# Performance work log

Measured on AMD Instinct MI355X. Metric: run time of the kernel, lower is better.

## Reference

```python
import jax, jax.numpy as jnp
import numpy as np

B = 4
C = 128           # input channels
H = W = 512       # image size
P = 16            # patch size
GH = GW = 32      # token grid (H//P, W//P)
N = GH * GW       # num patches = 1024
PATCH_DIM = C * P * P  # 32768
DIM = 512         # embed dim
MLP = 256         # ffn hidden
DH = 64           # dim per head
HEADS = (2, 4, 8) # per-layer head counts
NUM_REL = (2 * GH - 1) * (2 * GW - 1)  # 3969


def _rel_index():
    # faithful to the torch buffer construction (meshgrid default 'ij')
    coords = np.stack(np.meshgrid(np.arange(GH), np.arange(GW), indexing='ij')).reshape(2, -1)
    rc = (coords[:, :, None] - coords[:, None, :]).transpose(1, 2, 0)  # [N,N,2]
    rc[..., 0] += GH - 1
    rc[..., 1] += GW - 1
    rc[..., 0] *= 2 * GH - 1
    return jnp.asarray(rc.sum(-1))  # [N,N] int

REL_IDX = _rel_index()


def _ln(x, s, b):
    m = x.mean(-1, keepdims=True)
    v = x.var(-1, keepdims=True)
    return (x - m) / jnp.sqrt(v + 1e-5) * s + b


def setup_inputs() -> dict:
    key = jax.random.key(0)
    ks = iter(jax.random.split(key, 40))
    def rn(shape, scale=0.02):
        return jax.random.normal(next(ks), shape, jnp.float32) * scale
    inp = {"img": jax.random.normal(next(ks), (B, C, H, W), jnp.float32)}
    inp["patch_w"] = rn((PATCH_DIM, DIM))
    inp["patch_b"] = jnp.zeros((DIM,), jnp.float32)
    inp["pos_emb"] = rn((1, N, DIM), 1.0)
    inp["ln1_s"] = jnp.ones((3, DIM), jnp.float32)
    inp["ln1_b"] = jnp.zeros((3, DIM), jnp.float32)
    inp["ln2_s"] = jnp.ones((3, DIM), jnp.float32)
    inp["ln2_b"] = jnp.zeros((3, DIM), jnp.float32)
    for l, h in enumerate(HEADS):
        inner = DH * h
        inp[f"qkv_w{l}"] = rn((DIM, 3 * inner))
        inp[f"out_w{l}"] = rn((inner, DIM))
        inp[f"out_b{l}"] = jnp.zeros((DIM,), jnp.float32)
        inp[f"bias{l}"] = rn((NUM_REL, h))
    inp["ff_w1"] = rn((3, DIM, MLP))
    inp["ff_b1"] = jnp.zeros((3, MLP), jnp.float32)
    inp["ff_w2"] = rn((3, MLP, DIM))
    inp["ff_b2"] = jnp.zeros((3, DIM), jnp.float32)
    return inp


def reference(img, patch_w, patch_b, pos_emb, ln1_s, ln1_b, ln2_s, ln2_b,
              qkv_w0, qkv_w1, qkv_w2, out_w0, out_w1, out_w2,
              out_b0, out_b1, out_b2, bias0, bias1, bias2,
              ff_w1, ff_b1, ff_w2, ff_b2):
    b = img.shape[0]
    # Rearrange 'b c (h p1) (w p2) -> b (h w) (p1 p2 c)'
    x = img.reshape(b, C, GH, P, GW, P).transpose(0, 2, 4, 3, 5, 1).reshape(b, N, PATCH_DIM)
    x = x @ patch_w + patch_b + pos_emb

    qkv_ws = (qkv_w0, qkv_w1, qkv_w2)
    out_ws = (out_w0, out_w1, out_w2)
    out_bs = (out_b0, out_b1, out_b2)
    tables = (bias0, bias1, bias2)

    for l, h in enumerate(HEADS):
        # attention with relative position bias
        xn = _ln(x, ln1_s[l], ln1_b[l])
        qkv = xn @ qkv_ws[l]                                  # [b, N, 3*h*DH]
        q, k, v = jnp.split(qkv, 3, axis=-1)
        q = q.reshape(b, N, h, DH).transpose(0, 2, 1, 3)      # bhnd
        k = k.reshape(b, N, h, DH).transpose(0, 2, 1, 3)
        v = v.reshape(b, N, h, DH).transpose(0, 2, 1, 3)
        dots = jnp.einsum('bhnd,bhmd->bhnm', q, k) * (DH ** -0.5)
        rel = tables[l][REL_IDX].transpose(2, 0, 1)           # [h, N, N]
        attn = jax.nn.softmax(dots + rel[None], axis=-1)
        o = jnp.einsum('bhnm,bhmd->bhnd', attn, v)
        o = o.transpose(0, 2, 1, 3).reshape(b, N, h * DH)
        x = o @ out_ws[l] + out_bs[l] + x
        # feed-forward
        xn = _ln(x, ln2_s[l], ln2_b[l])
        hmid = jax.nn.gelu(xn @ ff_w1[l] + ff_b1[l], approximate=False)
        x = hmid @ ff_w2[l] + ff_b2[l] + x

    return x.transpose(0, 2, 1).reshape(b, DIM, GH, GW)
```

## Files before the change

### kernel.cpp

```cpp
#include <hip/hip_runtime.h>

typedef unsigned short u16;
typedef __bf16 bf16x8 __attribute__((ext_vector_type(8)));
typedef float f32x4 __attribute__((ext_vector_type(4)));

#define AS1 __attribute__((address_space(1)))
#define AS3 __attribute__((address_space(3)))
#define MFMA(a,b,c) __builtin_amdgcn_mfma_f32_16x16x32_bf16(a,b,c,0,0,0)

__device__ __forceinline__ u16 f2bf(float f) {
    union { float f; unsigned u; } x; x.f = f;
    unsigned r = x.u + 0x7fffu + ((x.u >> 16) & 1u);
    return (u16)(r >> 16);
}

__global__ void k_patch_wT(const float* __restrict__ w, u16* __restrict__ o)
{
    __shared__ u16 T[256*33];
    int c = blockIdx.x, n0 = blockIdx.y*32;
    int t = threadIdx.x;
    int rr = t >> 5, cc = t & 31;
    #pragma unroll
    for (int i = 0; i < 32; ++i) {
        int r = i*8 + rr;
        int k = (r >> 4)*2048 + (r & 15)*128 + c;
        T[r*33 + cc] = f2bf(w[(size_t)k*512 + n0 + cc]);
    }
    __syncthreads();
    #pragma unroll
    for (int i = 0; i < 4; ++i) {
        int j  = i*8 + (t >> 5);
        int ch = t & 31;
        union { u16 u[8]; uint4 v; } pk;
        #pragma unroll
        for (int q = 0; q < 8; ++q) pk.u[q] = T[(ch*8+q)*33 + j];
        *(uint4*)(o + (size_t)(n0 + j)*32768 + c*256 + ch*8) = pk.v;
    }
}

__global__ void k_init_x(float* __restrict__ x, const float* __restrict__ pb, const float* __restrict__ pe)
{
    int i4 = blockIdx.x*256 + threadIdx.x;
    size_t base = (size_t)i4*4;
    float4 a = *(const float4*)(pb + (base & 511));
    float4 b = *(const float4*)(pe + (base & 524287));
    float4 r = make_float4(a.x+b.x, a.y+b.y, a.z+b.z, a.w+b.w);
    *(float4*)(x + base) = r;
}

__global__ __launch_bounds__(1024) void k_patch_gemm(
    const float* __restrict__ img, const u16* __restrict__ Bt, float* __restrict__ Cf)
{
    __shared__ alignas(16) u16 As[2*128*64];
    __shared__ alignas(16) u16 Bs[2*512*64];
    const int t = threadIdx.x;
    const int bid = blockIdx.x;
    const int z = bid & 7;
    const int tile = bid >> 3;
    const int b = tile >> 3, gh0 = (tile & 7)*4;
    const int m0 = tile*128;
    const int wave = t >> 6, lane = t & 63;
    const int r16 = lane & 15, g = lane >> 4;
    const int wm = (wave >> 3)*64, wn = (wave & 7)*64;

    const int arow = t >> 6;
    const int ghl = arow >> 2, p1l = arow & 3;
    const int aw = (t & 63)*8;
    const int tok = ghl*32 + (aw >> 4);
    unsigned abyte = (unsigned)(tok*128 + p1l*32 + (aw & 15)*2);
    abyte ^= (unsigned)((tok & 7) << 4);
    const float* imgb = img + (size_t)b*128*262144
                      + (size_t)((gh0 + ghl)*16 + p1l)*512 + aw;
    const int brow = t >> 3;
    const int bchunk = (t & 7) ^ (brow & 7);
    const u16* Bb = Bt + (size_t)brow*32768 + (size_t)z*4096 + bchunk*8;
    u16* Bsd = Bs + t*8;

    f32x4 acc[4][4];
    const f32x4 zz = {0.f,0.f,0.f,0.f};
    #pragma unroll
    for (int im = 0; im < 4; ++im)
        #pragma unroll
        for (int in_ = 0; in_ < 4; ++in_) acc[im][in_] = zz;

#define STAGE(KC, BUF) do {                                                          \
    const int c_ = z*16 + ((KC) >> 2);                                               \
    const float* src_ = imgb + (size_t)c_*262144 + ((KC) & 3)*2048;                  \
    float4 a0_ = *(const float4*)src_;                                               \
    float4 a1_ = *(const float4*)(src_ + 4);                                         \
    _Pragma("unroll")                                                                \
    for (int i_ = 0; i_ < 4; ++i_)                                                   \
        __builtin_amdgcn_global_load_lds((AS1 void*)(Bb + (size_t)i_*128*32768 + (KC)*64), \
                                         (AS3 void*)(Bsd + (BUF)*32768 + i_*8192), 16, 0, 0); \
    union { u16 u[8]; uint4 v; } pk_;                                                \
    pk_.u[0]=f2bf(a0_.x); pk_.u[1]=f2bf(a0_.y); pk_.u[2]=f2bf(a0_.z); pk_.u[3]=f2bf(a0_.w); \
    pk_.u[4]=f2bf(a1_.x); pk_.u[5]=f2bf(a1_.y); pk_.u[6]=f2bf(a1_.z); pk_.u[7]=f2bf(a1_.w); \
    *(uint4*)((char*)As + (BUF)*16384 + abyte) = pk_.v;                              \
} while(0)

    STAGE(0, 0);
    __syncthreads();
    int cur = 0;
    for (int kc = 0; kc < 64; ++kc) {
        if (kc < 63) STAGE(kc + 1, cur ^ 1);
        const char* Asb = (const char*)As + cur*16384;
        const char* Bsb = (const char*)Bs + cur*65536;
        #pragma unroll
        for (int kk = 0; kk < 64; kk += 32) {
            bf16x8 af[4], bfr[4];
            #pragma unroll
            for (int im = 0; im < 4; ++im) {
                unsigned off = ((unsigned)((wm + im*16 + r16)*128 + kk*2 + g*16))
                             ^ (unsigned)((r16 & 7) << 4);
                af[im] = *(const bf16x8*)(Asb + off);
            }
            #pragma unroll
            for (int in_ = 0; in_ < 4; ++in_) {
                unsigned off = ((unsigned)((wn + in_*16 + r16)*128 + kk*2 + g*16))
                             ^ (unsigned)((r16 & 7) << 4);
                bfr[in_] = *(const bf16x8*)(Bsb + off);
            }
            #pragma unroll
            for (int im = 0; im < 4; ++im)
                #pragma unroll
                for (int in_ = 0; in_ < 4; ++in_)
                    acc[im][in_] = MFMA(af[im], bfr[in_], acc[im][in_]);
        }
        __syncthreads();
        cur ^= 1;
    }
#undef STAGE
    #pragma unroll
    for (int im = 0; im < 4; ++im) {
        int row = m0 + wm + im*16 + g*4;
        #pragma unroll
        for (int in_ = 0; in_ < 4; ++in_) {
            int col = wn + in_*16 + r16;
            #pragma unroll
            for (int r = 0; r < 4; ++r)
                __hip_atomic_fetch_add(&Cf[(size_t)(row + r)*512 + col], acc[im][in_][r],
                                       __ATOMIC_RELAXED, __HIP_MEMORY_SCOPE_AGENT);
        }
    }
}

__global__ void k_transpose_cvt(const float* __restrict__ in, u16* __restrict__ o, int K, int N)
{
    __shared__ float T[32*33];
    int kt = blockIdx.x*32, nt = blockIdx.y*32;
    int t = threadIdx.x, r = t >> 5, c = t & 31;
    #pragma unroll
    for (int i = 0; i < 4; ++i)
        T[(r + i*8)*33 + c] = in[(size_t)(kt + r + i*8)*N + nt + c];
    __syncthreads();
    #pragma unroll
    for (int i = 0; i < 4; ++i)
        o[(size_t)(nt + r + i*8)*K + kt + c] = f2bf(T[c*33 + r + i*8]);
}

__global__ void k_ln(const float* __restrict__ x, const float* __restrict__ sc,
                     const float* __restrict__ bi, u16* __restrict__ o)
{
    int row = blockIdx.x, lane = threadIdx.x;
    const float* xr = x + (size_t)row*512 + lane*8;
    float4 v0 = *(const float4*)xr;
    float4 v1 = *(const float4*)(xr + 4);
    float vv[8] = {v0.x,v0.y,v0.z,v0.w,v1.x,v1.y,v1.z,v1.w};
    float sum = 0.f, sq = 0.f;
    #pragma unroll
    for (int i = 0; i < 8; ++i) { sum += vv[i]; sq += vv[i]*vv[i]; }
    #pragma unroll
    for (int m = 1; m < 64; m <<= 1) { sum += __shfl_xor(sum, m, 64); sq += __shfl_xor(sq, m, 64); }
    float mean = sum * (1.f/512.f);
    float var  = sq  * (1.f/512.f) - mean*mean;
    float rstd = rsqrtf(var + 1e-5f);
    int d = lane*8;
    union { u16 u[8]; uint4 v; } pk;
    #pragma unroll
    for (int i = 0; i < 8; ++i) pk.u[i] = f2bf((vv[i]-mean)*rstd*sc[d+i] + bi[d+i]);
    *(uint4*)(o + (size_t)row*512 + d) = pk.v;
}

template<int EPI>
__global__ __launch_bounds__(256) void k_gemm(
    const u16* __restrict__ A, int lda,
    const u16* __restrict__ Bt, int ldb,
    int Kblk,
    float* __restrict__ Cf, u16* __restrict__ Cb, int ldc,
    const float* __restrict__ bias)
{
    __shared__ alignas(16) u16 As[128*64];
    __shared__ alignas(16) u16 Bs[128*64];
    const int t = threadIdx.x;
    const int m0 = blockIdx.x*128, n0 = blockIdx.y*128;
    const int kz = blockIdx.z*Kblk;
    const int wave = t >> 6, lane = t & 63;
    const int wm = (wave >> 1)*64, wn = (wave & 1)*64;
    const int r16 = lane & 15, g = lane >> 4;
    const u16* Ab = A + (size_t)(m0 + (t>>3))*lda + kz + (t&7)*8;
    const u16* Bb = Bt + (size_t)(n0 + (t>>3))*ldb + kz + (t&7)*8;
    u16* Asd = As + t*8;
    u16* Bsd = Bs + t*8;
    f32x4 acc[4][4];
    const f32x4 z4 = {0.f,0.f,0.f,0.f};
    #pragma unroll
    for (int im = 0; im < 4; ++im)
        #pragma unroll
        for (int in_ = 0; in_ < 4; ++in_) acc[im][in_] = z4;

    for (int k = 0; k < Kblk; k += 64) {
        #pragma unroll
        for (int i = 0; i < 4; ++i) {
            __builtin_amdgcn_global_load_lds((AS1 void*)(Ab + (size_t)i*32*lda + k), (AS3 void*)(Asd + i*2048), 16, 0, 0);
            __builtin_amdgcn_global_load_lds((AS1 void*)(Bb + (size_t)i*32*ldb + k), (AS3 void*)(Bsd + i*2048), 16, 0, 0);
        }
        __syncthreads();
        #pragma unroll
        for (int kk = 0; kk < 64; kk += 32) {
            bf16x8 af[4], bfr[4];
            #pragma unroll
            for (int im = 0; im < 4; ++im)
                af[im] = *(const bf16x8*)(As + (wm + im*16 + r16)*64 + kk + g*8);
            #pragma unroll
            for (int in_ = 0; in_ < 4; ++in_)
                bfr[in_] = *(const bf16x8*)(Bs + (wn + in_*16 + r16)*64 + kk + g*8);
            #pragma unroll
            for (int im = 0; im < 4; ++im)
                #pragma unroll
                for (int in_ = 0; in_ < 4; ++in_)
                    acc[im][in_] = MFMA(af[im], bfr[in_], acc[im][in_]);
        }
        __syncthreads();
    }
    #pragma unroll
    for (int im = 0; im < 4; ++im) {
        int row = m0 + wm + im*16 + g*4;
        #pragma unroll
        for (int in_ = 0; in_ < 4; ++in_) {
            int col = n0 + wn + in_*16 + r16;
            #pragma unroll
            for (int r = 0; r < 4; ++r) {
                float v = acc[im][in_][r];
                size_t idx = (size_t)(row + r)*ldc + col;
                if constexpr (EPI == 1) {
                    Cb[idx] = f2bf(v);
                } else if constexpr (EPI == 2) {
                    float xv = v + bias[col];
                    Cb[idx] = f2bf(0.5f*xv*(1.f + erff(xv*0.70710678118654752f)));
                } else {
                    Cf[idx] += v + bias[col];
                }
            }
        }
    }
}

__global__ __launch_bounds__(256) void k_attn(
    const u16* __restrict__ qkv, const float* __restrict__ bt,
    u16* __restrict__ o, int H)
{
    const int LD = 80;
    __shared__ alignas(16) u16 Qs[64*80], Ks[64*80], Vs[64*80];
    __shared__ alignas(16) u16 Ps[4][16*80];
    const int inner = H*64, s3 = 3*inner;
    const int qt = blockIdx.x, head = blockIdx.y, b = blockIdx.z;
    const int t = threadIdx.x, wave = t >> 6, lane = t & 63;
    const int r16 = lane & 15, g = lane >> 4;
    const int q0 = qt*64;
    const size_t tokbase = (size_t)b*1024;
    const int hoff = head*64;

    #pragma unroll
    for (int it = 0; it < 2; ++it) {
        int flat = it*256 + t, r = flat >> 3, d0 = (flat & 7)*8;
        uint4 v = *(const uint4*)(qkv + (tokbase + q0 + r)*s3 + hoff + d0);
        *(uint4*)(Qs + r*LD + d0) = v;
    }
    __syncthreads();
    bf16x8 aQ0 = *(const bf16x8*)(Qs + (wave*16 + r16)*LD + g*8);
    bf16x8 aQ1 = *(const bf16x8*)(Qs + (wave*16 + r16)*LD + 32 + g*8);

    float m_[4], l_[4];
    f32x4 O[4];
    const f32x4 z4 = {0.f,0.f,0.f,0.f};
    #pragma unroll
    for (int r = 0; r < 4; ++r) { m_[r] = -1e30f; l_[r] = 0.f; O[r] = z4; }
    const int qg_base = q0 + wave*16 + g*4;

    for (int kt = 0; kt < 16; ++kt) {
        const int key0 = kt*64;
        #pragma unroll
        for (int it = 0; it < 2; ++it) {
            int flat = it*256 + t, r = flat >> 3, d0 = (flat & 7)*8;
            uint4 v = *(const uint4*)(qkv + (tokbase + key0 + r)*s3 + inner + hoff + d0);
            *(uint4*)(Ks + r*LD + d0) = v;
        }
        #pragma unroll
        for (int it = 0; it < 2; ++it) {
            int flat = it*256 + t, key = flat & 63, d0 = (flat >> 6)*8;
            uint4 v = *(const uint4*)(qkv + (tokbase + key0 + key)*s3 + 2*inner + hoff + d0);
            const u16* pv = (const u16*)&v;
            #pragma unroll
            for (int i = 0; i < 8; ++i) Vs[(d0+i)*LD + key] = pv[i];
        }
        __syncthreads();

        float Sv[4][4];
        #pragma unroll
        for (int kb = 0; kb < 4; ++kb) {
            bf16x8 k0f = *(const bf16x8*)(Ks + (kb*16 + r16)*LD + g*8);
            bf16x8 k1f = *(const bf16x8*)(Ks + (kb*16 + r16)*LD + 32 + g*8);
            f32x4 S = z4;
            S = MFMA(aQ0, k0f, S);
            S = MFMA(aQ1, k1f, S);
            int keyg = key0 + kb*16 + r16;
            int kgh = keyg >> 5, kgw = keyg & 31;
            #pragma unroll
            for (int r = 0; r < 4; ++r) {
                int qg = qg_base + r;
                int rel = ((qg >> 5) - kgh + 31)*63 + ((qg & 31) - kgw + 31);
                Sv[kb][r] = S[r]*0.125f + bt[rel*H + head];
            }
        }
        float mx[4], al[4], ps[4];
        #pragma unroll
        for (int r = 0; r < 4; ++r)
            mx[r] = fmaxf(fmaxf(Sv[0][r], Sv[1][r]), fmaxf(Sv[2][r], Sv[3][r]));
        #pragma unroll
        for (int msk = 1; msk < 16; msk <<= 1)
            #pragma unroll
            for (int r = 0; r < 4; ++r) mx[r] = fmaxf(mx[r], __shfl_xor(mx[r], msk, 64));
        #pragma unroll
        for (int r = 0; r < 4; ++r) {
            float nm = fmaxf(m_[r], mx[r]);
            al[r] = __expf(m_[r] - nm);
            m_[r] = nm;
            ps[r] = 0.f;
        }
        #pragma unroll
        for (int kb = 0; kb < 4; ++kb)
            #pragma unroll
            for (int r = 0; r < 4; ++r) {
                float p = __expf(Sv[kb][r] - m_[r]);
                Sv[kb][r] = p;
                ps[r] += p;
            }
        #pragma unroll
        for (int msk = 1; msk < 16; msk <<= 1)
            #pragma unroll
            for (int r = 0; r < 4; ++r) ps[r] += __shfl_xor(ps[r], msk, 64);
        #pragma unroll
        for (int r = 0; r < 4; ++r) l_[r] = l_[r]*al[r] + ps[r];
        #pragma unroll
        for (int kb = 0; kb < 4; ++kb)
            #pragma unroll
            for (int r = 0; r < 4; ++r)
                Ps[wave][(g*4 + r)*LD + kb*16 + r16] = f2bf(Sv[kb][r]);
        #pragma unroll
        for (int dt = 0; dt < 4; ++dt)
            #pragma unroll
            for (int r = 0; r < 4; ++r) O[dt][r] = O[dt][r]*al[r];
        __syncthreads();
        bf16x8 aP0 = *(const bf16x8*)(Ps[wave] + r16*LD + g*8);
        bf16x8 aP1 = *(const bf16x8*)(Ps[wave] + r16*LD + 32 + g*8);
        #pragma unroll
        for (int dt = 0; dt < 4; ++dt) {
            bf16x8 v0 = *(const bf16x8*)(Vs + (dt*16 + r16)*LD + g*8);
            bf16x8 v1 = *(const bf16x8*)(Vs + (dt*16 + r16)*LD + 32 + g*8);
            O[dt] = MFMA(aP0, v0, O[dt]);
            O[dt] = MFMA(aP1, v1, O[dt]);
        }
        __syncthreads();
    }
    #pragma unroll
    for (int dt = 0; dt < 4; ++dt)
        #pragma unroll
        for (int r = 0; r < 4; ++r) {
            int token = q0 + wave*16 + g*4 + r;
            o[(tokbase + token)*inner + hoff + dt*16 + r16] = f2bf(O[dt][r] / l_[r]);
        }
}

__global__ void k_out_transpose(const float* __restrict__ x, float* __restrict__ o)
{
    __shared__ float T[32*33];
    int d0 = blockIdx.x*32, n0 = blockIdx.y*32, b = blockIdx.z;
    int t = threadIdx.x, r = t >> 5, c = t & 31;
    #pragma unroll
    for (int i = 0; i < 4; ++i)
        T[(r+i*8)*33 + c] = x[((size_t)b*1024 + n0 + r + i*8)*512 + d0 + c];
    __syncthreads();
    #pragma unroll
    for (int i = 0; i < 4; ++i)
        o[((size_t)b*512 + d0 + r + i*8)*1024 + n0 + c] = T[c*33 + (r+i*8)];
}

extern "C" void kernel_launch(void* const* d_in, const int* in_sizes, int n_in,
                              void* d_out, int out_size, void* d_ws, size_t ws_size,
                              hipStream_t stream)
{
    (void)in_sizes; (void)n_in; (void)out_size; (void)ws_size;
    const float* img     = (const float*)d_in[0];
    const float* patch_w = (const float*)d_in[1];
    const float* patch_b = (const float*)d_in[2];
    const float* pos_emb = (const float*)d_in[3];
    const float* ln1_s   = (const float*)d_in[4];
    const float* ln1_b   = (const float*)d_in[5];
    const float* ln2_s   = (const float*)d_in[6];
    const float* ln2_b   = (const float*)d_in[7];
    const float* qkv_w[3] = {(const float*)d_in[8],  (const float*)d_in[12], (const float*)d_in[16]};
    const float* out_w[3] = {(const float*)d_in[9],  (const float*)d_in[13], (const float*)d_in[17]};
    const float* out_b[3] = {(const float*)d_in[10], (const float*)d_in[14], (const float*)d_in[18]};
    const float* biasT[3] = {(const float*)d_in[11], (const float*)d_in[15], (const float*)d_in[19]};
    const float* ff_w1 = (const float*)d_in[20];
    const float* ff_b1 = (const float*)d_in[21];
    const float* ff_w2 = (const float*)d_in[22];
    const float* ff_b2 = (const float*)d_in[23];
    float* out = (float*)d_out;

    char* ws = (char*)d_ws;
    size_t off = 0;
    auto alloc = [&](size_t bytes) -> void* {
        void* p = ws + off; off += (bytes + 255) & ~(size_t)255; return p;
    };
    u16*   pwT  = (u16*)  alloc(512ull*32768*2);
    float* x    = (float*)alloc(4096ull*512*4);
    u16*   xn   = (u16*)  alloc(4096ull*512*2);
    u16*   qkv  = (u16*)  alloc(4096ull*1536*2);
    u16*   ob   = (u16*)  alloc(4096ull*512*2);
    u16*   mid  = (u16*)  alloc(4096ull*256*2);
    u16*   qkvT = (u16*)  alloc(1536ull*512*2);
    u16*   outT = (u16*)  alloc(512ull*512*2);
    u16*   f1T  = (u16*)  alloc(256ull*512*2);
    u16*   f2T  = (u16*)  alloc(512ull*256*2);

    k_patch_wT<<<dim3(128,16), 256, 0, stream>>>(patch_w, pwT);
    k_init_x<<<2048, 256, 0, stream>>>(x, patch_b, pos_emb);
    k_patch_gemm<<<256, 1024, 0, stream>>>(img, pwT, x);

    const int HS[3] = {2,4,8};
    for (int l = 0; l < 3; ++l) {
        int h = HS[l], inner = 64*h, n3 = 3*inner;
        k_transpose_cvt<<<dim3(16, n3/32),    256, 0, stream>>>(qkv_w[l], qkvT, 512, n3);
        k_transpose_cvt<<<dim3(inner/32, 16), 256, 0, stream>>>(out_w[l], outT, inner, 512);
        k_transpose_cvt<<<dim3(16, 8),        256, 0, stream>>>(ff_w1 + (size_t)l*512*256, f1T, 512, 256);
        k_transpose_cvt<<<dim3(8, 16),        256, 0, stream>>>(ff_w2 + (size_t)l*256*512, f2T, 256, 512);

        k_ln<<<4096, 64, 0, stream>>>(x, ln1_s + l*512, ln1_b + l*512, xn);
        k_gemm<1><<<dim3(32, n3/128), 256, 0, stream>>>(xn, 512, qkvT, 512, 512,
                                                        nullptr, qkv, n3, nullptr);
        k_attn<<<dim3(16, h, 4), 256, 0, stream>>>(qkv, biasT[l], ob, h);
        k_gemm<3><<<dim3(32, 4), 256, 0, stream>>>(ob, inner, outT, inner, inner,
                                                   x, nullptr, 512, out_b[l]);
        k_ln<<<4096, 64, 0, stream>>>(x, ln2_s + l*512, ln2_b + l*512, xn);
        k_gemm<2><<<dim3(32, 2), 256, 0, stream>>>(xn, 512, f1T, 512, 512,
                                                   nullptr, mid, 256, ff_b1 + l*256);
        k_gemm<3><<<dim3(32, 4), 256, 0, stream>>>(mid, 256, f2T, 256, 256,
                                                   x, nullptr, 512, ff_b2 + l*512);
    }
    k_out_transpose<<<dim3(16, 32, 4), 256, 0, stream>>>(x, out);
}
```

Baseline: 707.6 us.

## Batch weight transposes into one launch and software-pipeline patch GEMM loads

```diff
diff --git a/kernel.cpp b/kernel.cpp
--- a/kernel.cpp
+++ b/kernel.cpp
@@ -46,6 +46,30 @@
     float4 b = *(const float4*)(pe + (base & 524287));
     float4 r = make_float4(a.x+b.x, a.y+b.y, a.z+b.z, a.w+b.w);
     *(float4*)(x + base) = r;
+}
+
+struct TXJob { const float* in; u16* out; int K, N, tiles; };
+struct TXArgs { TXJob j[12]; };
+
+__global__ void k_wT_all(TXArgs a)
+{
+    __shared__ float T[32*33];
+    int bid = blockIdx.x;
+    int ji = 0;
+    while (bid >= a.j[ji].tiles) { bid -= a.j[ji].tiles; ++ji; }
+    const float* __restrict__ in = a.j[ji].in;
+    u16* __restrict__ o = a.j[ji].out;
+    const int K = a.j[ji].K, N = a.j[ji].N;
+    const int tn = N >> 5;
+    const int kt = (bid / tn) * 32, nt = (bid % tn) * 32;
+    int t = threadIdx.x, r = t >> 5, c = t & 31;
+    #pragma unroll
+    for (int i = 0; i < 4; ++i)
+        T[(r + i*8)*33 + c] = in[(size_t)(kt + r + i*8)*N + nt + c];
+    __syncthreads();
+    #pragma unroll
+    for (int i = 0; i < 4; ++i)
+        o[(size_t)(nt + r + i*8)*K + kt + c] = f2bf(T[c*33 + r + i*8]);
 }
 
 __global__ __launch_bounds__(1024) void k_patch_gemm(
@@ -83,28 +107,25 @@
         #pragma unroll
         for (int in_ = 0; in_ < 4; ++in_) acc[im][in_] = zz;
 
-#define STAGE(KC, BUF) do {                                                          \
+    float4 e0, e1, o0, o1;
+
+#define ALOAD(R0, R1, KC) do {                                                       \
     const int c_ = z*16 + ((KC) >> 2);                                               \
-    const float* src_ = imgb + (size_t)c_*262144 + ((KC) & 3)*2048;                  \
-    float4 a0_ = *(const float4*)src_;                                               \
-    float4 a1_ = *(const float4*)(src_ + 4);                                         \
-    _Pragma("unroll")                                                                \
+    const float* s_ = imgb + (size_t)c_*262144 + ((KC) & 3)*2048;                    \
+    R0 = *(const float4*)s_;  R1 = *(const float4*)(s_ + 4); } while(0)
+#define AWRITE(R0, R1, BUF) do {                                                     \
+    union { u16 u[8]; uint4 v; } pk_;                                                \
+    pk_.u[0]=f2bf(R0.x); pk_.u[1]=f2bf(R0.y); pk_.u[2]=f2bf(R0.z); pk_.u[3]=f2bf(R0.w); \
+    pk_.u[4]=f2bf(R1.x); pk_.u[5]=f2bf(R1.y); pk_.u[6]=f2bf(R1.z); pk_.u[7]=f2bf(R1.w); \
+    *(uint4*)((char*)As + (BUF)*16384 + abyte) = pk_.v; } while(0)
+#define BSTAGE(KC, BUF) do { _Pragma("unroll")                                       \
     for (int i_ = 0; i_ < 4; ++i_)                                                   \
         __builtin_amdgcn_global_load_lds((AS1 void*)(Bb + (size_t)i_*128*32768 + (KC)*64), \
-                                         (AS3 void*)(Bsd + (BUF)*32768 + i_*8192), 16, 0, 0); \
-    union { u16 u[8]; uint4 v; } pk_;                                                \
-    pk_.u[0]=f2bf(a0_.x); pk_.u[1]=f2bf(a0_.y); pk_.u[2]=f2bf(a0_.z); pk_.u[3]=f2bf(a0_.w); \
-    pk_.u[4]=f2bf(a1_.x); pk_.u[5]=f2bf(a1_.y); pk_.u[6]=f2bf(a1_.z); pk_.u[7]=f2bf(a1_.w); \
-    *(uint4*)((char*)As + (BUF)*16384 + abyte) = pk_.v;                              \
-} while(0)
-
-    STAGE(0, 0);
-    __syncthreads();
-    int cur = 0;
-    for (int kc = 0; kc < 64; ++kc) {
-        if (kc < 63) STAGE(kc + 1, cur ^ 1);
-        const char* Asb = (const char*)As + cur*16384;
-        const char* Bsb = (const char*)Bs + cur*65536;
+                                         (AS3 void*)(Bsd + (BUF)*32768 + i_*8192), 16, 0, 0); } while(0)
+
+    auto compute = [&](int buf) {
+        const char* Asb = (const char*)As + buf*16384;
+        const char* Bsb = (const char*)Bs + buf*65536;
         #pragma unroll
         for (int kk = 0; kk < 64; kk += 32) {
             bf16x8 af[4], bfr[4];
@@ -126,10 +147,27 @@
                 for (int in_ = 0; in_ < 4; ++in_)
                     acc[im][in_] = MFMA(af[im], bfr[in_], acc[im][in_]);
         }
-        __syncthreads();
-        cur ^= 1;
-    }
-#undef STAGE
+    };
+
+    ALOAD(e0, e1, 0);
+    BSTAGE(0, 0);
+    AWRITE(e0, e1, 0);
+    ALOAD(o0, o1, 1);
+    __syncthreads();
+    for (int kc = 0; kc < 64; kc += 2) {
+        if (kc + 2 < 64) ALOAD(e0, e1, kc + 2);
+        AWRITE(o0, o1, 1);
+        BSTAGE(kc + 1, 1);
+        compute(0);
+        __syncthreads();
+        if (kc + 3 < 64) ALOAD(o0, o1, kc + 3);
+        if (kc + 2 < 64) { AWRITE(e0, e1, 0); BSTAGE(kc + 2, 0); }
+        compute(1);
+        __syncthreads();
+    }
+#undef ALOAD
+#undef AWRITE
+#undef BSTAGE
     #pragma unroll
     for (int im = 0; im < 4; ++im) {
         int row = m0 + wm + im*16 + g*4;
@@ -142,20 +180,6 @@
                                        __ATOMIC_RELAXED, __HIP_MEMORY_SCOPE_AGENT);
         }
     }
-}
-
-__global__ void k_transpose_cvt(const float* __restrict__ in, u16* __restrict__ o, int K, int N)
-{
-    __shared__ float T[32*33];
-    int kt = blockIdx.x*32, nt = blockIdx.y*32;
-    int t = threadIdx.x, r = t >> 5, c = t & 31;
-    #pragma unroll
-    for (int i = 0; i < 4; ++i)
-        T[(r + i*8)*33 + c] = in[(size_t)(kt + r + i*8)*N + nt + c];
-    __syncthreads();
-    #pragma unroll
-    for (int i = 0; i < 4; ++i)
-        o[(size_t)(nt + r + i*8)*K + kt + c] = f2bf(T[c*33 + r + i*8]);
 }
 
 __global__ void k_ln(const float* __restrict__ x, const float* __restrict__ sc,
@@ -181,11 +205,10 @@
     *(uint4*)(o + (size_t)row*512 + d) = pk.v;
 }
 
-template<int EPI>
+template<int EPI, int KB>
 __global__ __launch_bounds__(256) void k_gemm(
     const u16* __restrict__ A, int lda,
     const u16* __restrict__ Bt, int ldb,
-    int Kblk,
     float* __restrict__ Cf, u16* __restrict__ Cb, int ldc,
     const float* __restrict__ bias)
 {
@@ -193,12 +216,11 @@
     __shared__ alignas(16) u16 Bs[128*64];
     const int t = threadIdx.x;
     const int m0 = blockIdx.x*128, n0 = blockIdx.y*128;
-    const int kz = blockIdx.z*Kblk;
     const int wave = t >> 6, lane = t & 63;
     const int wm = (wave >> 1)*64, wn = (wave & 1)*64;
     const int r16 = lane & 15, g = lane >> 4;
-    const u16* Ab = A + (size_t)(m0 + (t>>3))*lda + kz + (t&7)*8;
-    const u16* Bb = Bt + (size_t)(n0 + (t>>3))*ldb + kz + (t&7)*8;
+    const u16* Ab = A + (size_t)(m0 + (t>>3))*lda + (t&7)*8;
+    const u16* Bb = Bt + (size_t)(n0 + (t>>3))*ldb + (t&7)*8;
     u16* Asd = As + t*8;
     u16* Bsd = Bs + t*8;
     f32x4 acc[4][4];
@@ -208,7 +230,8 @@
         #pragma unroll
         for (int in_ = 0; in_ < 4; ++in_) acc[im][in_] = z4;
 
-    for (int k = 0; k < Kblk; k += 64) {
+    #pragma unroll
+    for (int k = 0; k < KB; k += 64) {
         #pragma unroll
         for (int i = 0; i < 4; ++i) {
             __builtin_amdgcn_global_load_lds((AS1 void*)(Ab + (size_t)i*32*lda + k), (AS3 void*)(Asd + i*2048), 16, 0, 0);
@@ -418,6 +441,8 @@
     const float* ff_b2 = (const float*)d_in[23];
     float* out = (float*)d_out;
 
+    const int HS[3] = {2, 4, 8};
+
     char* ws = (char*)d_ws;
     size_t off = 0;
     auto alloc = [&](size_t bytes) -> void* {
@@ -429,34 +454,54 @@
     u16*   qkv  = (u16*)  alloc(4096ull*1536*2);
     u16*   ob   = (u16*)  alloc(4096ull*512*2);
     u16*   mid  = (u16*)  alloc(4096ull*256*2);
-    u16*   qkvT = (u16*)  alloc(1536ull*512*2);
-    u16*   outT = (u16*)  alloc(512ull*512*2);
-    u16*   f1T  = (u16*)  alloc(256ull*512*2);
-    u16*   f2T  = (u16*)  alloc(512ull*256*2);
+    u16*   qkvT = (u16*)  alloc(2688ull*512*2);
+    u16*   outT = (u16*)  alloc(512ull*896*2);
+    u16*   f1T  = (u16*)  alloc(3ull*256*512*2);
+    u16*   f2T  = (u16*)  alloc(3ull*512*256*2);
+
+    u16* qkvT_l[3] = { qkvT, qkvT + 384ull*512, qkvT + (384ull+768)*512 };
+    u16* outT_l[3] = { outT, outT + 512ull*128, outT + 512ull*(128+256) };
+    u16* f1T_l[3]  = { f1T,  f1T  + 256ull*512, f1T  + 2ull*256*512 };
+    u16* f2T_l[3]  = { f2T,  f2T  + 512ull*256, f2T  + 2ull*512*256 };
 
     k_patch_wT<<<dim3(128,16), 256, 0, stream>>>(patch_w, pwT);
     k_init_x<<<2048, 256, 0, stream>>>(x, patch_b, pos_emb);
+
+    TXArgs tx;
+    int tj = 0, total_tiles = 0;
+    auto add_job = [&](const float* in, u16* o, int K, int N) {
+        tx.j[tj] = TXJob{in, o, K, N, (K/32)*(N/32)};
+        total_tiles += tx.j[tj].tiles; ++tj;
+    };
+    for (int l = 0; l < 3; ++l) add_job(qkv_w[l], qkvT_l[l], 512, 3*64*HS[l]);
+    for (int l = 0; l < 3; ++l) add_job(out_w[l], outT_l[l], 64*HS[l], 512);
+    for (int l = 0; l < 3; ++l) add_job(ff_w1 + (size_t)l*512*256, f1T_l[l], 512, 256);
+    for (int l = 0; l < 3; ++l) add_job(ff_w2 + (size_t)l*256*512, f2T_l[l], 256, 512);
+    k_wT_all<<<total_tiles, 256, 0, stream>>>(tx);
+
     k_patch_gemm<<<256, 1024, 0, stream>>>(img, pwT, x);
 
-    const int HS[3] = {2,4,8};
     for (int l = 0; l < 3; ++l) {
         int h = HS[l], inner = 64*h, n3 = 3*inner;
-        k_transpose_cvt<<<dim3(16, n3/32),    256, 0, stream>>>(qkv_w[l], qkvT, 512, n3);
-        k_transpose_cvt<<<dim3(inner/32, 16), 256, 0, stream>>>(out_w[l], outT, inner, 512);
-        k_transpose_cvt<<<dim3(16, 8),        256, 0, stream>>>(ff_w1 + (size_t)l*512*256, f1T, 512, 256);
-        k_transpose_cvt<<<dim3(8, 16),        256, 0, stream>>>(ff_w2 + (size_t)l*256*512, f2T, 256, 512);
 
         k_ln<<<4096, 64, 0, stream>>>(x, ln1_s + l*512, ln1_b + l*512, xn);
-        k_gemm<1><<<dim3(32, n3/128), 256, 0, stream>>>(xn, 512, qkvT, 512, 512,
-                                                        nullptr, qkv, n3, nullptr);
+        k_gemm<1,512><<<dim3(32, n3/128), 256, 0, stream>>>(xn, 512, qkvT_l[l], 512,
+                                                            nullptr, qkv, n3, nullptr);
         k_attn<<<dim3(16, h, 4), 256, 0, stream>>>(qkv, biasT[l], ob, h);
-        k_gemm<3><<<dim3(32, 4), 256, 0, stream>>>(ob, inner, outT, inner, inner,
-                                                   x, nullptr, 512, out_b[l]);
+        if (l == 0)
+            k_gemm<3,128><<<dim3(32, 4), 256, 0, stream>>>(ob, inner, outT_l[l], inner,
+                                                           x, nullptr, 512, out_b[l]);
+        else if (l == 1)
+            k_gemm<3,256><<<dim3(32, 4), 256, 0, stream>>>(ob, inner, outT_l[l], inner,
+                                                           x, nullptr, 512, out_b[l]);
+        else
+            k_gemm<3,512><<<dim3(32, 4), 256, 0, stream>>>(ob, inner, outT_l[l], inner,
+                                                           x, nullptr, 512, out_b[l]);
         k_ln<<<4096, 64, 0, stream>>>(x, ln2_s + l*512, ln2_b + l*512, xn);
-        k_gemm<2><<<dim3(32, 2), 256, 0, stream>>>(xn, 512, f1T, 512, 512,
-                                                   nullptr, mid, 256, ff_b1 + l*256);
-        k_gemm<3><<<dim3(32, 4), 256, 0, stream>>>(mid, 256, f2T, 256, 256,
-                                                   x, nullptr, 512, ff_b2 + l*512);
+        k_gemm<2,512><<<dim3(32, 2), 256, 0, stream>>>(xn, 512, f1T_l[l], 512,
+                                                       nullptr, mid, 256, ff_b1 + l*256);
+        k_gemm<3,256><<<dim3(32, 4), 256, 0, stream>>>(mid, 256, f2T_l[l], 256,
+                                                       x, nullptr, 512, ff_b2 + l*512);
     }
     k_out_transpose<<<dim3(16, 32, 4), 256, 0, stream>>>(x, out);
 }
```

After: 940.4 us. 1.33x slower.
